# Performance work log

Measured on AMD Instinct MI355X. Metric: run time of the kernel, lower is better.

The kernel has to match this reference:

```python
import jax, jax.numpy as jnp
import numpy as np

DIM = 192
HEADS = 4
B, H, W = 2, 256, 256
EPS = 1e-12  # torch F.normalize default eps


def setup_inputs() -> dict:
    key = jax.random.key(0)
    ks = jax.random.split(key, 6)
    x = jax.random.normal(ks[0], (B, DIM, H, W), jnp.float32)
    mask = jax.random.uniform(ks[1], (B, 1, 1, H * W), jnp.float32)
    w_qkv = jax.random.normal(ks[2], (3 * DIM, DIM, 1, 1), jnp.float32) * 0.05
    w_dw = jax.random.normal(ks[3], (3 * DIM, 1, 3, 3), jnp.float32) * 0.05
    w_proj = jax.random.normal(ks[4], (DIM, DIM, 1, 1), jnp.float32) * 0.05
    temperature = jnp.ones((HEADS, 1, 1), jnp.float32)
    return {"x": x, "mask": mask, "w_qkv": w_qkv, "w_dw": w_dw,
            "w_proj": w_proj, "temperature": temperature}


def reference(x, mask, w_qkv, w_dw, w_proj, temperature):
    b, c, h, w = x.shape
    ch = c // HEADS  # channels per head
    # 1x1 conv -> pointwise matmul over channels
    qkv = jnp.einsum('bchw,oc->bohw', x, w_qkv[:, :, 0, 0])
    # depthwise 3x3 conv, padding=1
    qkv = jax.lax.conv_general_dilated(
        qkv, w_dw, window_strides=(1, 1), padding='SAME',
        dimension_numbers=('NCHW', 'OIHW', 'NCHW'),
        feature_group_count=3 * c)
    q, k, v = jnp.split(qkv, 3, axis=1)
    rs = lambda t: t.reshape(b, HEADS, ch, h * w)  # b head c (h w)
    q, k, v = rs(q), rs(k), rs(v)
    l2n = lambda t: t / jnp.maximum(
        jnp.linalg.norm(t, axis=-1, keepdims=True), EPS)
    q = l2n(q) * mask
    k = l2n(k) * mask
    # channel-wise (transposed) attention: (b,h,c,c)
    attn = jnp.einsum('bhcn,bhdn->bhcd', q, k) * temperature
    attn = jax.nn.softmax(attn, axis=-1)
    out = jnp.einsum('bhcd,bhdn->bhcn', attn, v).reshape(b, c, h, w)
    out = jnp.einsum('bchw,oc->bohw', out, w_proj[:, :, 0, 0])
    return out
```

## Files before the change

kernel.cpp:

```cpp
#include <hip/hip_runtime.h>

#define NP 65536
#define EPSF 1e-12f

#define OFF_PRE   0L
#define OFF_VDW   12582912L
#define OFF_GRAMP 25165824L
#define OFF_NQKP  27525120L
#define OFF_GRAM  27623424L
#define OFF_NRM   27632640L
#define OFF_M     27633024L
#define WS_NEED_FLOATS 27669888L

__global__ __launch_bounds__(256) void gemm_cn(
    const float* __restrict__ A,
    const float* __restrict__ X,
    float* __restrict__ Out)
{
    const int px0 = blockIdx.x * 128;
    const int oc0 = blockIdx.y * 64;
    const int tid = threadIdx.x;
    const int tx = tid & 31;
    const int ty = tid >> 5;

    __shared__ float As[16][68];
    __shared__ float Xs[16][132];

    float acc[8][4];
    #pragma unroll
    for (int i = 0; i < 8; i++)
        #pragma unroll
        for (int j = 0; j < 4; j++) acc[i][j] = 0.f;

    for (int kb = 0; kb < 192; kb += 16) {
        {
            int oc = tid >> 2;
            int k0 = (tid & 3) * 4;
            const float4 av = *(const float4*)&A[(long)(oc0 + oc) * 192 + kb + k0];
            As[k0 + 0][oc] = av.x;
            As[k0 + 1][oc] = av.y;
            As[k0 + 2][oc] = av.z;
            As[k0 + 3][oc] = av.w;
        }
        {
            int r = tid >> 4;
            int f4 = tid & 15;
            const float* xrow = &X[(long)(kb + r) * NP + px0];
            *(float4*)&Xs[r][f4 * 4]      = *(const float4*)&xrow[f4 * 4];
            *(float4*)&Xs[r][64 + f4 * 4] = *(const float4*)&xrow[64 + f4 * 4];
        }
        __syncthreads();
        #pragma unroll
        for (int k = 0; k < 16; k++) {
            float4 a0 = *(const float4*)&As[k][ty * 8];
            float4 a1 = *(const float4*)&As[k][ty * 8 + 4];
            float4 xv = *(const float4*)&Xs[k][tx * 4];
            float av[8] = {a0.x, a0.y, a0.z, a0.w, a1.x, a1.y, a1.z, a1.w};
            float xl[4] = {xv.x, xv.y, xv.z, xv.w};
            #pragma unroll
            for (int i = 0; i < 8; i++)
                #pragma unroll
                for (int j = 0; j < 4; j++)
                    acc[i][j] = fmaf(av[i], xl[j], acc[i][j]);
        }
        __syncthreads();
    }
    #pragma unroll
    for (int i = 0; i < 8; i++) {
        float4 o4 = make_float4(acc[i][0], acc[i][1], acc[i][2], acc[i][3]);
        *(float4*)&Out[(long)(oc0 + ty * 8 + i) * NP + px0 + tx * 4] = o4;
    }
}

__global__ __launch_bounds__(256) void dwgram_k(
    const float* __restrict__ pre, const float* __restrict__ wdw,
    const float* __restrict__ mask,
    float* __restrict__ gramP, float* __restrict__ nqkp)
{
    const int y = blockIdx.x;
    const int h = blockIdx.y;
    const int t = threadIdx.x;
    const int g = t >> 6;
    const int u = t & 63;
    const int ti = u >> 3, tj = u & 7;

    __shared__ float qs[48][132];
    __shared__ float ks[48][132];
    __shared__ float4 m2s4[32];

    float acc[6][6];
    #pragma unroll
    for (int a = 0; a < 6; a++)
        #pragma unroll
        for (int d = 0; d < 6; d++) acc[a][d] = 0.f;

    float nsum = 0.f;
    const int col4 = t & 31;
    const int rgrp = t >> 5;

    for (int s = 0; s < 2; s++) {
        const int x0 = s * 128 + col4 * 4;
        if (t < 32) {
            float4 mv = *(const float4*)&mask[y * 256 + s * 128 + t * 4];
            m2s4[t] = make_float4(mv.x * mv.x, mv.y * mv.y,
                                  mv.z * mv.z, mv.w * mv.w);
        }
        #pragma unroll
        for (int iL = 0; iL < 6; iL++) {
            const int r = rgrp + 8 * iL;
            #pragma unroll
            for (int side = 0; side < 2; side++) {
                const int ch = side ? (192 + h * 48 + r) : (h * 48 + r);
                const float* src = pre + (long)ch * NP + y * 256;
                const float* wp = wdw + ch * 9;
                float in3[3][6];
                #pragma unroll
                for (int dy = 0; dy < 3; dy++) {
                    const int yy = y + dy - 1;
                    const bool rv = (yy >= 0) && (yy < 256);
                    const float* rp = src + (dy - 1) * 256;
                    #pragma unroll
                    for (int uu = 0; uu < 6; uu++) {
                        const int xx = x0 + uu - 1;
                        in3[dy][uu] = (rv && xx >= 0 && xx < 256) ? rp[xx] : 0.f;
                    }
                }
                float o[4];
                #pragma unroll
                for (int q = 0; q < 4; q++) {
                    float sa = 0.f;
                    #pragma unroll
                    for (int dy = 0; dy < 3; dy++)
                        #pragma unroll
                        for (int dx = 0; dx < 3; dx++)
                            sa = fmaf(in3[dy][q + dx], wp[dy * 3 + dx], sa);
                    o[q] = sa;
                }
                float* dst = side ? &ks[r][col4 * 4] : &qs[r][col4 * 4];
                *(float4*)dst = make_float4(o[0], o[1], o[2], o[3]);
            }
        }
        __syncthreads();
        #pragma unroll
        for (int p = 0; p < 32; p += 4) {
            const int pp = 32 * g + p;
            const float4 m2 = m2s4[pp >> 2];
            float4 qm[6];
            #pragma unroll
            for (int a = 0; a < 6; a++) {
                float4 qv = *(const float4*)&qs[6 * ti + a][pp];
                qm[a] = make_float4(qv.x * m2.x, qv.y * m2.y,
                                    qv.z * m2.z, qv.w * m2.w);
            }
            #pragma unroll
            for (int d = 0; d < 6; d++) {
                const float4 kv = *(const float4*)&ks[6 * tj + d][pp];
                #pragma unroll
                for (int a = 0; a < 6; a++) {
                    acc[a][d] = fmaf(qm[a].x, kv.x, acc[a][d]);
                    acc[a][d] = fmaf(qm[a].y, kv.y, acc[a][d]);
                    acc[a][d] = fmaf(qm[a].z, kv.z, acc[a][d]);
                    acc[a][d] = fmaf(qm[a].w, kv.w, acc[a][d]);
                }
            }
        }
        if (t < 96) {
            const float* row = (t < 48) ? &qs[t][0] : &ks[t - 48][0];
            #pragma unroll 8
            for (int p = 0; p < 128; p += 4) {
                float4 v = *(const float4*)&row[p];
                nsum = fmaf(v.x, v.x, nsum);
                nsum = fmaf(v.y, v.y, nsum);
                nsum = fmaf(v.z, v.z, nsum);
                nsum = fmaf(v.w, v.w, nsum);
            }
        }
        __syncthreads();
    }
    if (t < 96) {
        const int gch = (t < 48) ? (h * 48 + t) : (192 + h * 48 + (t - 48));
        nqkp[gch * 256 + y] = nsum;
    }
    float* scratch = &qs[0][0];
    for (int gg = 0; gg < 4; gg++) {
        if (g == gg) {
            #pragma unroll
            for (int a = 0; a < 6; a++)
                #pragma unroll
                for (int d = 0; d < 6; d++) {
                    const int idx = (6 * ti + a) * 48 + 6 * tj + d;
                    if (gg == 0) scratch[idx] = acc[a][d];
                    else scratch[idx] += acc[a][d];
                }
        }
        __syncthreads();
    }
    float* gp = gramP + ((long)y * 4 + h) * 2304;
    for (int idx = t; idx < 2304; idx += 256) gp[idx] = scratch[idx];
}

__global__ __launch_bounds__(256) void dwv_k(
    const float* __restrict__ vpre, const float* __restrict__ wdw,
    float* __restrict__ vdw)
{
    const int c = blockIdx.y;
    const int y = blockIdx.x;
    const int x = threadIdx.x;
    const float* p = vpre + (long)c * NP + y * 256 + x;
    const float* wp = wdw + (384 + c) * 9;
    float s = 0.f;
    int ii = 0;
    #pragma unroll
    for (int dy = -1; dy <= 1; dy++)
        #pragma unroll
        for (int dx = -1; dx <= 1; dx++, ii++) {
            int yy = y + dy, xx = x + dx;
            float v = (yy >= 0 && yy < 256 && xx >= 0 && xx < 256)
                          ? p[dy * 256 + dx] : 0.f;
            s = fmaf(v, wp[ii], s);
        }
    vdw[(long)c * NP + y * 256 + x] = s;
}

__global__ __launch_bounds__(256) void reduce_k(
    const float* __restrict__ gramP, const float* __restrict__ nqkp,
    float* __restrict__ gram, float* __restrict__ nrm)
{
    int idx = blockIdx.x * 256 + threadIdx.x;
    if (idx < 9216) {
        const float* p = gramP + idx;
        float s = 0.f;
        #pragma unroll 8
        for (int blk = 0; blk < 256; blk++) s += p[(long)blk * 9216];
        gram[idx] = s;
    } else if (idx < 9600) {
        int i2 = idx - 9216;
        const float* p = nqkp + (long)i2 * 256;
        float s = 0.f;
        #pragma unroll 8
        for (int r = 0; r < 256; r++) s += p[r];
        nrm[i2] = s;
    }
}

__global__ __launch_bounds__(256) void finalize_k(
    const float* __restrict__ gram, const float* __restrict__ nrm,
    const float* __restrict__ wproj, const float* __restrict__ temp,
    float* __restrict__ M)
{
    int h = blockIdx.x;
    int t = threadIdx.x;
    __shared__ float attn[48][49];
    __shared__ float qn[48], kn[48];
    if (t < 96) {
        int c = t % 48;
        int ch = h * 48 + c;
        float v = nrm[(t < 48 ? 0 : 192) + ch];
        float s = fmaxf(sqrtf(v), EPSF);
        if (t < 48) qn[c] = s; else kn[c] = s;
    }
    __syncthreads();
    float tp = temp[h];
    for (int idx = t; idx < 2304; idx += 256) {
        int c = idx / 48, d = idx % 48;
        attn[c][d] = gram[(h * 48 + c) * 48 + d] * tp / (qn[c] * kn[d]);
    }
    __syncthreads();
    if (t < 48) {
        float mx = -1e30f;
        for (int d = 0; d < 48; d++) mx = fmaxf(mx, attn[t][d]);
        float s = 0.f;
        for (int d = 0; d < 48; d++) {
            float e = expf(attn[t][d] - mx);
            attn[t][d] = e; s += e;
        }
        float inv = 1.f / s;
        for (int d = 0; d < 48; d++) attn[t][d] *= inv;
    }
    __syncthreads();
    for (int idx = t; idx < 9216; idx += 256) {
        int o = idx / 48, d = idx % 48;
        float s = 0.f;
        #pragma unroll
        for (int c = 0; c < 48; c++)
            s = fmaf(wproj[o * 192 + h * 48 + c], attn[c][d], s);
        M[o * 192 + h * 48 + d] = s;
    }
}

extern "C" void kernel_launch(void* const* d_in, const int* in_sizes, int n_in,
                              void* d_out, int out_size, void* d_ws, size_t ws_size,
                              hipStream_t stream) {
    const float* x     = (const float*)d_in[0];
    const float* mask  = (const float*)d_in[1];
    const float* wqkv  = (const float*)d_in[2];
    const float* wdw   = (const float*)d_in[3];
    const float* wproj = (const float*)d_in[4];
    const float* temp  = (const float*)d_in[5];
    float* out = (float*)d_out;
    float* ws  = (float*)d_ws;

    if (ws_size < (size_t)WS_NEED_FLOATS * sizeof(float)) return;

    float* pre   = ws + OFF_PRE;
    float* vdw   = ws + OFF_VDW;
    float* gramP = ws + OFF_GRAMP;
    float* nqkp  = ws + OFF_NQKP;
    float* gram  = ws + OFF_GRAM;
    float* nrm   = ws + OFF_NRM;
    float* Mbuf  = ws + OFF_M;

    for (int b = 0; b < 2; b++) {
        const float* xb    = x    + (long)b * 192 * NP;
        const float* maskb = mask + (long)b * NP;
        float*       outb  = out  + (long)b * 192 * NP;

        gemm_cn<<<dim3(512, 6, 1), 256, 0, stream>>>(wqkv, xb, pre);
        dwgram_k<<<dim3(256, 4, 1), 256, 0, stream>>>(
            pre, wdw, maskb, gramP, nqkp);
        reduce_k<<<38, 256, 0, stream>>>(gramP, nqkp, gram, nrm);
        finalize_k<<<4, 256, 0, stream>>>(gram, nrm, wproj, temp, Mbuf);
        gemm_cn<<<dim3(512, 3, 1), 256, 0, stream>>>(wqkv + 384 * 192, xb, pre);
        dwv_k<<<dim3(256, 192, 1), 256, 0, stream>>>(pre, wdw, vdw);
        gemm_cn<<<dim3(512, 3, 1), 256, 0, stream>>>(Mbuf, vdw, outb);
    }
}
```

Measured before the change: 1.405 ms.

## Use split-bf16 MFMA for pointwise GEMMs and stage depthwise halo in LDS

Replaces the FP32 FMA pointwise-conv GEMM with a bf16 MFMA GEMM. Each fp32 value is split into high and low bf16 parts and three MFMA products are summed, keeping close to fp32 accuracy. Weights are pre-packed once per launch and the projection matrix is emitted pre-packed. The depthwise+gram kernel now stages a 3-row halo per 8-channel group in shared memory instead of doing redundant global loads, and gets an occupancy hint. The costs are more MFMA work, per-element split packing of X inside the GEMM, extra synchronisation, and a small accuracy difference from the three-term approximation.

```diff
diff --git a/kernel.cpp b/kernel.cpp
--- a/kernel.cpp
+++ b/kernel.cpp
@@ -2,6 +2,9 @@
 
 #define NP 65536
 #define EPSF 1e-12f
+
+typedef __attribute__((ext_vector_type(8))) short s16x8;
+typedef __attribute__((ext_vector_type(4))) float f32x4;
 
 #define OFF_PRE   0L
 #define OFF_VDW   12582912L
@@ -10,69 +13,126 @@
 #define OFF_GRAM  27623424L
 #define OFF_NRM   27632640L
 #define OFF_M     27633024L
-#define WS_NEED_FLOATS 27669888L
-
-__global__ __launch_bounds__(256) void gemm_cn(
-    const float* __restrict__ A,
+#define OFF_WPK   27669888L
+#define WS_NEED_FLOATS 27780480L
+
+__device__ inline unsigned bf16rne(float x) {
+    unsigned u = __float_as_uint(x);
+    return (u + 0x7fffu + ((u >> 16) & 1u)) >> 16;
+}
+__device__ inline unsigned pksplit(float x) {
+    unsigned h = bf16rne(x);
+    unsigned hif = h << 16;
+    float r = x - __uint_as_float(hif);
+    unsigned l = bf16rne(r) & 0xffffu;
+    return hif | l;
+}
+__device__ inline void unpack8(uint4 p0, uint4 p1, s16x8& h, s16x8& l) {
+    union { unsigned u[4]; s16x8 v; } H, L;
+    H.u[0] = __builtin_amdgcn_perm(p0.y, p0.x, 0x07060302);
+    H.u[1] = __builtin_amdgcn_perm(p0.w, p0.z, 0x07060302);
+    H.u[2] = __builtin_amdgcn_perm(p1.y, p1.x, 0x07060302);
+    H.u[3] = __builtin_amdgcn_perm(p1.w, p1.z, 0x07060302);
+    L.u[0] = __builtin_amdgcn_perm(p0.y, p0.x, 0x05040100);
+    L.u[1] = __builtin_amdgcn_perm(p0.w, p0.z, 0x05040100);
+    L.u[2] = __builtin_amdgcn_perm(p1.y, p1.x, 0x05040100);
+    L.u[3] = __builtin_amdgcn_perm(p1.w, p1.z, 0x05040100);
+    h = H.v; l = L.v;
+}
+
+__global__ __launch_bounds__(256) void packw_k(
+    const float* __restrict__ w, unsigned* __restrict__ wpk, int n)
+{
+    int i = blockIdx.x * 256 + threadIdx.x;
+    if (i < n) wpk[i] = pksplit(w[i]);
+}
+
+__global__ __launch_bounds__(256) void gemm_split(
+    const unsigned* __restrict__ Apk,
     const float* __restrict__ X,
     float* __restrict__ Out)
 {
-    const int px0 = blockIdx.x * 128;
+    __shared__ unsigned As[64][36];
+    __shared__ unsigned Xs[256][36];
+
+    const int t = threadIdx.x;
+    const int px0 = blockIdx.x * 256;
     const int oc0 = blockIdx.y * 64;
-    const int tid = threadIdx.x;
-    const int tx = tid & 31;
-    const int ty = tid >> 5;
-
-    __shared__ float As[16][68];
-    __shared__ float Xs[16][132];
-
-    float acc[8][4];
+    const int w = t >> 6;
+    const int l = t & 63;
+    const int lr = l & 15;
+    const int lq = l >> 4;
+
+    f32x4 acc[4][4];
     #pragma unroll
-    for (int i = 0; i < 8; i++)
-        #pragma unroll
-        for (int j = 0; j < 4; j++) acc[i][j] = 0.f;
-
-    for (int kb = 0; kb < 192; kb += 16) {
+    for (int m = 0; m < 4; m++)
+        #pragma unroll
+        for (int n = 0; n < 4; n++)
+            acc[m][n] = (f32x4){0.f, 0.f, 0.f, 0.f};
+
+    for (int ks = 0; ks < 6; ks++) {
+        const int k0 = ks * 32;
+        __syncthreads();
         {
-            int oc = tid >> 2;
-            int k0 = (tid & 3) * 4;
-            const float4 av = *(const float4*)&A[(long)(oc0 + oc) * 192 + kb + k0];
-            As[k0 + 0][oc] = av.x;
-            As[k0 + 1][oc] = av.y;
-            As[k0 + 2][oc] = av.z;
-            As[k0 + 3][oc] = av.w;
+            const int row = t >> 2, ch = (t & 3) * 8;
+            const unsigned* gp = Apk + (long)(oc0 + row) * 192 + k0 + ch;
+            uint4 a0 = *(const uint4*)gp;
+            uint4 a1 = *(const uint4*)(gp + 4);
+            *(uint4*)&As[row][ch] = a0;
+            *(uint4*)&As[row][ch + 4] = a1;
         }
         {
-            int r = tid >> 4;
-            int f4 = tid & 15;
-            const float* xrow = &X[(long)(kb + r) * NP + px0];
-            *(float4*)&Xs[r][f4 * 4]      = *(const float4*)&xrow[f4 * 4];
-            *(float4*)&Xs[r][64 + f4 * 4] = *(const float4*)&xrow[64 + f4 * 4];
-        }
-        __syncthreads();
-        #pragma unroll
-        for (int k = 0; k < 16; k++) {
-            float4 a0 = *(const float4*)&As[k][ty * 8];
-            float4 a1 = *(const float4*)&As[k][ty * 8 + 4];
-            float4 xv = *(const float4*)&Xs[k][tx * 4];
-            float av[8] = {a0.x, a0.y, a0.z, a0.w, a1.x, a1.y, a1.z, a1.w};
-            float xl[4] = {xv.x, xv.y, xv.z, xv.w};
-            #pragma unroll
-            for (int i = 0; i < 8; i++)
-                #pragma unroll
-                for (int j = 0; j < 4; j++)
-                    acc[i][j] = fmaf(av[i], xl[j], acc[i][j]);
-        }
-        __syncthreads();
+            const float* xp = X + (long)k0 * NP + px0 + t;
+            #pragma unroll
+            for (int j4 = 0; j4 < 8; j4++) {
+                uint4 v;
+                v.x = pksplit(xp[(long)(j4 * 4 + 0) * NP]);
+                v.y = pksplit(xp[(long)(j4 * 4 + 1) * NP]);
+                v.z = pksplit(xp[(long)(j4 * 4 + 2) * NP]);
+                v.w = pksplit(xp[(long)(j4 * 4 + 3) * NP]);
+                *(uint4*)&Xs[t][j4 * 4] = v;
+            }
+        }
+        __syncthreads();
+        s16x8 Ah[4], Al[4];
+        #pragma unroll
+        for (int m = 0; m < 4; m++) {
+            const unsigned* ap = &As[m * 16 + lr][lq * 8];
+            uint4 p0 = *(const uint4*)ap;
+            uint4 p1 = *(const uint4*)(ap + 4);
+            unpack8(p0, p1, Ah[m], Al[m]);
+        }
+        #pragma unroll
+        for (int n = 0; n < 4; n++) {
+            const unsigned* xp2 = &Xs[w * 64 + n * 16 + lr][lq * 8];
+            uint4 p0 = *(const uint4*)xp2;
+            uint4 p1 = *(const uint4*)(xp2 + 4);
+            s16x8 Xh, Xl;
+            unpack8(p0, p1, Xh, Xl);
+            #pragma unroll
+            for (int m = 0; m < 4; m++) {
+                acc[m][n] = __builtin_amdgcn_mfma_f32_16x16x32_bf16(
+                    Ah[m], Xh, acc[m][n], 0, 0, 0);
+                acc[m][n] = __builtin_amdgcn_mfma_f32_16x16x32_bf16(
+                    Ah[m], Xl, acc[m][n], 0, 0, 0);
+                acc[m][n] = __builtin_amdgcn_mfma_f32_16x16x32_bf16(
+                    Al[m], Xh, acc[m][n], 0, 0, 0);
+            }
+        }
     }
     #pragma unroll
-    for (int i = 0; i < 8; i++) {
-        float4 o4 = make_float4(acc[i][0], acc[i][1], acc[i][2], acc[i][3]);
-        *(float4*)&Out[(long)(oc0 + ty * 8 + i) * NP + px0 + tx * 4] = o4;
-    }
-}
-
-__global__ __launch_bounds__(256) void dwgram_k(
+    for (int m = 0; m < 4; m++)
+        #pragma unroll
+        for (int n = 0; n < 4; n++) {
+            float* op = Out + (long)(oc0 + m * 16 + lq * 4) * NP
+                        + px0 + w * 64 + n * 16 + lr;
+            #pragma unroll
+            for (int r = 0; r < 4; r++)
+                op[(long)r * NP] = acc[m][n][r];
+        }
+}
+
+__global__ __launch_bounds__(256, 2) void dwgram_k(
     const float* __restrict__ pre, const float* __restrict__ wdw,
     const float* __restrict__ mask,
     float* __restrict__ gramP, float* __restrict__ nqkp)
@@ -86,6 +146,7 @@
 
     __shared__ float qs[48][132];
     __shared__ float ks[48][132];
+    __shared__ float halo[8][3][132];
     __shared__ float4 m2s4[32];
 
     float acc[6][6];
@@ -96,48 +157,55 @@
 
     float nsum = 0.f;
     const int col4 = t & 31;
-    const int rgrp = t >> 5;
-
+    const int rL = t >> 5;
+
+    #pragma unroll 1
     for (int s = 0; s < 2; s++) {
-        const int x0 = s * 128 + col4 * 4;
+        const int x0 = s * 128;
         if (t < 32) {
-            float4 mv = *(const float4*)&mask[y * 256 + s * 128 + t * 4];
+            float4 mv = *(const float4*)&mask[y * 256 + x0 + t * 4];
             m2s4[t] = make_float4(mv.x * mv.x, mv.y * mv.y,
                                   mv.z * mv.z, mv.w * mv.w);
         }
-        #pragma unroll
-        for (int iL = 0; iL < 6; iL++) {
-            const int r = rgrp + 8 * iL;
-            #pragma unroll
-            for (int side = 0; side < 2; side++) {
-                const int ch = side ? (192 + h * 48 + r) : (h * 48 + r);
-                const float* src = pre + (long)ch * NP + y * 256;
+        #pragma unroll 1
+        for (int grp = 0; grp < 12; grp++) {
+            const int side = grp >= 6;
+            const int r0 = (grp % 6) * 8;
+            const int chBase = (side ? 192 : 0) + h * 48 + r0;
+            __syncthreads();
+            for (int idx = t; idx < 8 * 3 * 132; idx += 256) {
+                const int hc = idx / 396;
+                const int rem = idx - hc * 396;
+                const int dy = rem / 132;
+                const int col = rem - dy * 132;
+                const int yy = y + dy - 1;
+                const int xx = x0 + col - 1;
+                float v = 0.f;
+                if (yy >= 0 && yy < 256 && xx >= 0 && xx < 256)
+                    v = pre[(long)(chBase + hc) * NP + yy * 256 + xx];
+                halo[hc][dy][col] = v;
+            }
+            __syncthreads();
+            {
+                const int ch = chBase + rL;
                 const float* wp = wdw + ch * 9;
-                float in3[3][6];
+                const int c0 = col4 * 4;
+                float o0 = 0.f, o1 = 0.f, o2 = 0.f, o3 = 0.f;
                 #pragma unroll
                 for (int dy = 0; dy < 3; dy++) {
-                    const int yy = y + dy - 1;
-                    const bool rv = (yy >= 0) && (yy < 256);
-                    const float* rp = src + (dy - 1) * 256;
-                    #pragma unroll
-                    for (int uu = 0; uu < 6; uu++) {
-                        const int xx = x0 + uu - 1;
-                        in3[dy][uu] = (rv && xx >= 0 && xx < 256) ? rp[xx] : 0.f;
-                    }
+                    const float* hp = &halo[rL][dy][c0];
+                    const float w0 = wp[dy * 3 + 0];
+                    const float w1 = wp[dy * 3 + 1];
+                    const float w2 = wp[dy * 3 + 2];
+                    float i0 = hp[0], i1 = hp[1], i2 = hp[2];
+                    float i3 = hp[3], i4 = hp[4], i5 = hp[5];
+                    o0 = fmaf(i0, w0, o0); o0 = fmaf(i1, w1, o0); o0 = fmaf(i2, w2, o0);
+                    o1 = fmaf(i1, w0, o1); o1 = fmaf(i2, w1, o1); o1 = fmaf(i3, w2, o1);
+                    o2 = fmaf(i2, w0, o2); o2 = fmaf(i3, w1, o2); o2 = fmaf(i4, w2, o2);
+                    o3 = fmaf(i3, w0, o3); o3 = fmaf(i4, w1, o3); o3 = fmaf(i5, w2, o3);
                 }
-                float o[4];
-                #pragma unroll
-                for (int q = 0; q < 4; q++) {
-                    float sa = 0.f;
-                    #pragma unroll
-                    for (int dy = 0; dy < 3; dy++)
-                        #pragma unroll
-                        for (int dx = 0; dx < 3; dx++)
-                            sa = fmaf(in3[dy][q + dx], wp[dy * 3 + dx], sa);
-                    o[q] = sa;
-                }
-                float* dst = side ? &ks[r][col4 * 4] : &qs[r][col4 * 4];
-                *(float4*)dst = make_float4(o[0], o[1], o[2], o[3]);
+                float* dst = side ? &ks[r0 + rL][c0] : &qs[r0 + rL][c0];
+                *(float4*)dst = make_float4(o0, o1, o2, o3);
             }
         }
         __syncthreads();
@@ -246,7 +314,7 @@
 __global__ __launch_bounds__(256) void finalize_k(
     const float* __restrict__ gram, const float* __restrict__ nrm,
     const float* __restrict__ wproj, const float* __restrict__ temp,
-    float* __restrict__ M)
+    unsigned* __restrict__ Mpk)
 {
     int h = blockIdx.x;
     int t = threadIdx.x;
@@ -284,7 +352,7 @@
         #pragma unroll
         for (int c = 0; c < 48; c++)
             s = fmaf(wproj[o * 192 + h * 48 + c], attn[c][d], s);
-        M[o * 192 + h * 48 + d] = s;
+        Mpk[o * 192 + h * 48 + d] = pksplit(s);
     }
 }
 
@@ -302,26 +370,30 @@
 
     if (ws_size < (size_t)WS_NEED_FLOATS * sizeof(float)) return;
 
-    float* pre   = ws + OFF_PRE;
-    float* vdw   = ws + OFF_VDW;
-    float* gramP = ws + OFF_GRAMP;
-    float* nqkp  = ws + OFF_NQKP;
-    float* gram  = ws + OFF_GRAM;
-    float* nrm   = ws + OFF_NRM;
-    float* Mbuf  = ws + OFF_M;
+    float*    pre   = ws + OFF_PRE;
+    float*    vdw   = ws + OFF_VDW;
+    float*    gramP = ws + OFF_GRAMP;
+    float*    nqkp  = ws + OFF_NQKP;
+    float*    gram  = ws + OFF_GRAM;
+    float*    nrm   = ws + OFF_NRM;
+    unsigned* mpk   = (unsigned*)(ws + OFF_M);
+    unsigned* wpk   = (unsigned*)(ws + OFF_WPK);
+
+    packw_k<<<432, 256, 0, stream>>>(wqkv, wpk, 576 * 192);
 
     for (int b = 0; b < 2; b++) {
         const float* xb    = x    + (long)b * 192 * NP;
         const float* maskb = mask + (long)b * NP;
         float*       outb  = out  + (long)b * 192 * NP;
 
-        gemm_cn<<<dim3(512, 6, 1), 256, 0, stream>>>(wqkv, xb, pre);
+        gemm_split<<<dim3(256, 6, 1), 256, 0, stream>>>(wpk, xb, pre);
         dwgram_k<<<dim3(256, 4, 1), 256, 0, stream>>>(
             pre, wdw, maskb, gramP, nqkp);
         reduce_k<<<38, 256, 0, stream>>>(gramP, nqkp, gram, nrm);
-        finalize_k<<<4, 256, 0, stream>>>(gram, nrm, wproj, temp, Mbuf);
-        gemm_cn<<<dim3(512, 3, 1), 256, 0, stream>>>(wqkv + 384 * 192, xb, pre);
+        finalize_k<<<4, 256, 0, stream>>>(gram, nrm, wproj, temp, mpk);
+        gemm_split<<<dim3(256, 3, 1), 256, 0, stream>>>(
+            wpk + 384 * 192, xb, pre);
         dwv_k<<<dim3(256, 192, 1), 256, 0, stream>>>(pre, wdw, vdw);
-        gemm_cn<<<dim3(512, 3, 1), 256, 0, stream>>>(Mbuf, vdw, outb);
-    }
-}
+        gemm_split<<<dim3(256, 3, 1), 256, 0, stream>>>(mpk, vdw, outb);
+    }
+}
```

Result: slower. 1.618 ms (+15.2%).
